# Kernel optimization log

Hardware: AMD Instinct MI355X
Metric: run time of the kernel (lower is better)

Reference implementation:

```python
import jax, jax.numpy as jnp
import numpy as np

N = 40000
IN_DIM = 2000
HID = 512
OUT_DIM = 30
E = 400000


def setup_inputs() -> dict:
    key = jax.random.key(0)
    k1, k2, k3, k4, k5, k6 = jax.random.split(key, 6)
    features = jax.random.normal(k1, (N, IN_DIM), dtype=jnp.float32)
    edge_index = jax.random.randint(k2, (2, E), 0, N, dtype=jnp.int64)
    # xavier_normal_(gain=1.414): std = gain * sqrt(2/(fan_in+fan_out))
    W1 = jax.random.normal(k3, (IN_DIM, HID), dtype=jnp.float32) * (1.414 * np.sqrt(2.0 / (IN_DIM + HID)))
    W2 = jax.random.normal(k4, (HID, OUT_DIM), dtype=jnp.float32) * (1.414 * np.sqrt(2.0 / (HID + OUT_DIM)))
    att_src = jax.random.normal(k5, (HID,), dtype=jnp.float32) * (1.414 * np.sqrt(2.0 / (1 + HID)))
    att_dst = jax.random.normal(k6, (HID,), dtype=jnp.float32) * (1.414 * np.sqrt(2.0 / (1 + HID)))
    return {"features": features, "W1": W1, "W2": W2,
            "att_src": att_src, "att_dst": att_dst, "edge_index": edge_index}


def _gat_propagate(x_proj, alpha_src, alpha_dst, src, dst, n_nodes):
    """GATConv message+aggregate (heads=1, aggr='add').
    x_proj: [N, C] projected features; alpha_src/alpha_dst: [N] per-node scores.
    """
    score = jax.nn.sigmoid(alpha_src[src] + alpha_dst[dst])          # [E]
    # segment softmax over destination neighborhoods (PyG softmax)
    seg_max = jax.ops.segment_max(score, dst, num_segments=n_nodes)  # [N]
    e = jnp.exp(score - seg_max[dst])                                # [E]
    seg_sum = jax.ops.segment_sum(e, dst, num_segments=n_nodes)     # [N]
    alpha = e / (seg_sum[dst] + 1e-16)                               # [E]
    msg = x_proj[src] * alpha[:, None]                               # [E, C] gather + scale
    return jax.ops.segment_sum(msg, dst, num_segments=n_nodes)      # [N, C] scatter-add


def _stagate_forward(features, W1, W2, att_src, att_dst, src, dst):
    n = features.shape[0]
    # conv1: attention=True (computes its own alpha)
    x1 = features @ W1                                # [N, HID]
    a_src = x1 @ att_src                              # [N]
    a_dst = x1 @ att_dst                              # [N]
    h1 = jax.nn.elu(_gat_propagate(x1, a_src, a_dst, src, dst, n))
    # conv2: attention=False -> just linear projection (heads=1 mean)
    h2 = h1 @ W2                                      # [N, OUT_DIM]
    # conv3: weights tied to W2^T, attention tied to conv1's alphas
    x3 = h2 @ W2.T                                    # [N, HID]
    h3 = jax.nn.elu(_gat_propagate(x3, a_src, a_dst, src, dst, n))
    # conv4: attention=False, weights tied to W1^T
    h4 = h3 @ W1.T                                    # [N, IN_DIM]
    return h2, h4


def reference(features, W1, W2, att_src, att_dst, edge_index):
    src = edge_index[0]
    dst = edge_index[1]
    return _stagate_forward(features, W1, W2, att_src, att_dst, src, dst)
```

## Files before the change

kernel.cpp:

```cpp
#include <hip/hip_runtime.h>
#include <cstdint>

#define NNODES 40000
#define INDIM 2000
#define HIDD 512
#define ODIM 30
#define NEDGES 400000
#define KPAD 2048

typedef short bf16x8 __attribute__((ext_vector_type(8)));
typedef float f32x4 __attribute__((ext_vector_type(4)));

__device__ __forceinline__ float bf2f(ushort u){ union{unsigned int i; float f;} x; x.i = ((unsigned int)u)<<16; return x.f; }
__device__ __forceinline__ ushort f2bf(float v){ union{float f; unsigned int u;} x; x.f=v; unsigned int r = x.u + 0x7fffu + ((x.u>>16)&1u); return (ushort)(r>>16); }

__device__ __forceinline__ int xcd_swz(int orig, int nwg){
  int q = nwg >> 3, r = nwg & 7;
  int xcd = orig & 7;
  int idx = orig >> 3;
  return (xcd < r ? xcd*(q+1) : r*(q+1) + (xcd-r)*q) + idx;
}

#define SB_FEAT   40000
#define SB_W1     (SB_FEAT + 4000)
#define SB_W2     (SB_W1 + 64)
#define SB_HIST   (SB_W2 + 1563)
#define SB_PAD    (SB_HIST + 96)
#define SB_CUR    (SB_PAD + 157)

__global__ __launch_bounds__(256) void setup_kernel(
    const float* __restrict__ features, const float* __restrict__ W1, const float* __restrict__ W2,
    const int* __restrict__ edst,
    ushort* __restrict__ featb, ushort* __restrict__ W1b, ushort* __restrict__ W1t,
    ushort* __restrict__ W2p, ushort* __restrict__ W2tc,
    int* __restrict__ deg, int* __restrict__ cursor){
  int b = blockIdx.x, t = threadIdx.x;
  if (b < SB_FEAT){
    int c = b*256 + t;
    int row = c >> 8, kc = c & 255;
    bf16x8 o;
    if (kc < INDIM/8) {
      const float* p = features + (size_t)row*INDIM + kc*8;
      #pragma unroll
      for (int j=0;j<8;++j) o[j] = (short)f2bf(p[j]);
    } else {
      #pragma unroll
      for (int j=0;j<8;++j) o[j] = 0;
    }
    *(bf16x8*)(featb + (size_t)row*KPAD + kc*8) = o;
  } else if (b < SB_W1){
    int idx = (b - SB_FEAT)*256 + t;
    int r = idx >> 9, c = idx & 511;
    ushort bb = f2bf(W1[idx]);
    W1b[idx] = bb;
    W1t[(size_t)c*KPAD + r] = bb;
  } else if (b < SB_W2){
    int idx = (b - SB_W1)*256 + t;
    int k = idx >> 5, c = idx & 31;
    float val = (c < ODIM) ? W2[k*ODIM + c] : 0.f;
    ushort bb = f2bf(val);
    W2p[k*32 + c] = bb;
    W2tc[c*HIDD + k] = bb;
  } else if (b < SB_HIST){
    int e = (b - SB_W2)*256 + t;
    if (e < NEDGES) atomicAdd(&deg[edst[e]], 1);
  } else if (b < SB_PAD){
    int z = (b - SB_HIST)*256 + t;
    int c = z / 48, r = 2000 + (z - c*48);
    W1t[(size_t)c*KPAD + r] = 0;
  } else {
    int z = (b - SB_PAD)*256 + t;
    if (z < NNODES) cursor[z] = 0;
  }
}

#define P_MID  asm volatile("" ::: "memory"); __builtin_amdgcn_s_barrier(); \
               asm volatile("s_waitcnt lgkmcnt(0)" ::: "memory"); \
               __builtin_amdgcn_sched_barrier(0); __builtin_amdgcn_s_setprio(1);
#define P_END  __builtin_amdgcn_s_setprio(0); asm volatile("" ::: "memory"); \
               __builtin_amdgcn_s_barrier(); __builtin_amdgcn_sched_barrier(0);
#define P_ENDW __builtin_amdgcn_s_setprio(0); \
               asm volatile("s_waitcnt vmcnt(4)" ::: "memory"); \
               asm volatile("" ::: "memory"); __builtin_amdgcn_s_barrier(); \
               __builtin_amdgcn_sched_barrier(0);

template<typename OutT, bool DOSCAN>
__global__ __launch_bounds__(512, 2) void gemm8_kernel(
    const ushort* __restrict__ A, const ushort* __restrict__ Bt,
    OutT* __restrict__ C, int M, int N, int K, int ldc, int nwg, int cshift,
    const int* __restrict__ degp, int* __restrict__ row_ptr)
{
  __shared__ __align__(16) char smem[131072];
  if constexpr (DOSCAN){
    if ((int)blockIdx.x == nwg){
      int* part = (int*)smem;
      const int t = threadIdx.x;
      const int base = t * 80;
      int s = 0;
      for (int j=0;j<80;++j){ int i = base+j; s += (i < NNODES) ? degp[i] : 0; }
      part[t] = s;
      __syncthreads();
      for (int off=1; off<512; off<<=1){
        int x = (t >= off) ? part[t-off] : 0;
        __syncthreads();
        part[t] += x;
        __syncthreads();
      }
      int run = (t > 0) ? part[t-1] : 0;
      for (int j=0;j<80;++j){
        int i = base+j;
        if (i <= NNODES){
          row_ptr[i] = run;
          if (i < NNODES) run += degp[i];
        }
      }
      return;
    }
  }
  ushort* Al = (ushort*)smem;
  ushort* Bl = (ushort*)(smem + 65536);
  const int tid = threadIdx.x;
  const int lane = tid & 63;
  const int w = tid >> 6;
  const int wm = w >> 2, wn = w & 3;
  const int s = xcd_swz(blockIdx.x, nwg);
  const int row0 = (s >> cshift) << 8;
  const int col0 = (s & ((1 << cshift) - 1)) << 8;
  const int NT = K >> 6;

  f32x4 acc[8][4] = {};
  bf16x8 a[4][2], b[4][2];

  auto stage = [&](bool isA, int kt, int h){
    const ushort* G = isA ? A : Bt;
    int base = isA ? row0 : col0;
    int lim  = isA ? M : N;
    ushort* L = (isA ? Al : Bl) + ((kt & 1) << 14);
    if (kt >= NT) kt -= NT;
    #pragma unroll
    for (int it = 0; it < 2; ++it){
      int ch = tid + (it << 9);
      int rl = (h << 7) + (ch >> 3);
      int cs = ch & 7;
      int gr = base + rl; gr = gr < lim ? gr : lim - 1;
      int gc = (kt << 6) + ((cs ^ (rl & 7)) << 3);
      __builtin_amdgcn_global_load_lds(
        (const __attribute__((address_space(1))) unsigned int*)(G + (size_t)gr*K + gc),
        (__attribute__((address_space(3))) unsigned int*)(L + rl*64 + cs*8), 16, 0, 0);
    }
  };
  auto lda = [&](int buf, int mf, int kk) -> bf16x8 {
    int rl = wm*128 + mf*16 + (lane & 15);
    int ko = kk*32 + ((lane >> 4) << 3);
    return *(const bf16x8*)&Al[(buf << 14) + rl*64 + (ko ^ ((rl & 7) << 3))];
  };
  auto ldb = [&](int buf, int nf, int kk) -> bf16x8 {
    int rl = wn*64 + nf*16 + (lane & 15);
    int ko = kk*32 + ((lane >> 4) << 3);
    return *(const bf16x8*)&Bl[(buf << 14) + rl*64 + (ko ^ ((rl & 7) << 3))];
  };
  auto mfma_q = [&](int mbase, int nbase){
    #pragma unroll
    for (int i=0;i<4;++i)
      #pragma unroll
      for (int j=0;j<2;++j)
        #pragma unroll
        for (int kk=0;kk<2;++kk)
          acc[mbase+i][nbase+j] = __builtin_amdgcn_mfma_f32_16x16x32_bf16(
              a[i][kk], b[nbase+j][kk], acc[mbase+i][nbase+j], 0, 0, 0);
  };

  stage(false, 0, 0); stage(false, 0, 1);
  stage(true , 0, 0); stage(true , 0, 1);
  stage(false, 1, 0); stage(false, 1, 1);
  asm volatile("s_waitcnt vmcnt(4)" ::: "memory");
  asm volatile("" ::: "memory");
  __builtin_amdgcn_s_barrier();
  __builtin_amdgcn_sched_barrier(0);

  const int NT2 = NT >> 1;
  for (int t = 0; t < NT2; ++t){
    const int kt0 = 2*t, kt1 = 2*t + 1;
    #pragma unroll
    for (int i=0;i<4;++i){ a[i][0]=lda(0,i,0); a[i][1]=lda(0,i,1); }
    #pragma unroll
    for (int j=0;j<2;++j){ b[j][0]=ldb(0,j,0); b[j][1]=ldb(0,j,1); }
    stage(true, kt1, 0);
    P_MID; mfma_q(0,0); P_END;
    #pragma unroll
    for (int j=2;j<4;++j){ b[j][0]=ldb(0,j,0); b[j][1]=ldb(0,j,1); }
    stage(true, kt1, 1);
    P_MID; mfma_q(0,2); P_END;
    #pragma unroll
    for (int i=0;i<4;++i){ a[i][0]=lda(0,4+i,0); a[i][1]=lda(0,4+i,1); }
    stage(false, kt0+2, 0);
    P_MID; mfma_q(4,0); P_END;
    stage(false, kt0+2, 1);
    P_MID; mfma_q(4,2); P_ENDW;
    #pragma unroll
    for (int i=0;i<4;++i){ a[i][0]=lda(1,i,0); a[i][1]=lda(1,i,1); }
    #pragma unroll
    for (int j=0;j<2;++j){ b[j][0]=ldb(1,j,0); b[j][1]=ldb(1,j,1); }
    stage(true, kt0+2, 0);
    P_MID; mfma_q(0,0); P_END;
    #pragma unroll
    for (int j=2;j<4;++j){ b[j][0]=ldb(1,j,0); b[j][1]=ldb(1,j,1); }
    stage(true, kt0+2, 1);
    P_MID; mfma_q(0,2); P_END;
    #pragma unroll
    for (int i=0;i<4;++i){ a[i][0]=lda(1,4+i,0); a[i][1]=lda(1,4+i,1); }
    stage(false, kt1+2, 0);
    P_MID; mfma_q(4,0); P_END;
    stage(false, kt1+2, 1);
    P_MID; mfma_q(4,2); P_ENDW;
  }

  asm volatile("s_waitcnt vmcnt(0)" ::: "memory");
  __syncthreads();

  if constexpr (sizeof(OutT)==2) {
    ushort* cs = (ushort*)smem;
    #pragma unroll
    for (int p=0;p<2;++p){
      if (wm == p){
        #pragma unroll
        for (int mf=0;mf<8;++mf)
          #pragma unroll
          for (int nf=0;nf<4;++nf)
            #pragma unroll
            for (int reg=0;reg<4;++reg)
              cs[(mf*16 + ((lane>>4)<<2) + reg)*264 + wn*64 + nf*16 + (lane&15)] = f2bf(acc[mf][nf][reg]);
      }
      __syncthreads();
      #pragma unroll
      for (int it=0; it<8; ++it){
        int ch = tid + it*512;
        int r = ch >> 5, c8 = (ch & 31) * 8;
        int gr = row0 + p*128 + r;
        if (gr < M && col0 + c8 + 8 <= N)
          *(bf16x8*)&((ushort*)C)[(size_t)gr*ldc + col0 + c8] = *(const bf16x8*)&cs[r*264 + c8];
      }
      __syncthreads();
    }
  } else {
    float* cf = (float*)smem;
    #pragma unroll
    for (int p=0;p<4;++p){
      if (wm == (p>>1)){
        int mh = (p & 1) * 4;
        #pragma unroll
        for (int i=0;i<4;++i)
          #pragma unroll
          for (int nf=0;nf<4;++nf)
            #pragma unroll
            for (int reg=0;reg<4;++reg)
              cf[(i*16 + ((lane>>4)<<2) + reg)*260 + wn*64 + nf*16 + (lane&15)] = acc[mh+i][nf][reg];
      }
      __syncthreads();
      #pragma unroll
      for (int it=0; it<8; ++it){
        int ch = tid + it*512;
        int r = ch >> 6, c4 = (ch & 63) * 4;
        int gr = row0 + p*64 + r, gc = col0 + c4;
        if (gr < M && gc + 4 <= N)
          *(f32x4*)&((float*)C)[(size_t)gr*ldc + gc] = *(const f32x4*)&cf[r*260 + c4];
      }
      __syncthreads();
    }
  }
}

#define PB_PLACE 1563
__global__ __launch_bounds__(256) void place_a_kernel(
    const int* __restrict__ esrc, const int* __restrict__ edst,
    const int* __restrict__ row_ptr, int* __restrict__ cursor, int* __restrict__ csr_src,
    const ushort* __restrict__ x1, const float* __restrict__ att_src, const float* __restrict__ att_dst,
    float* __restrict__ a_src, float* __restrict__ a_dst){
  int b = blockIdx.x, t = threadIdx.x;
  if (b < PB_PLACE){
    int e = b*256 + t;
    if (e >= NEDGES) return;
    int d = edst[e];
    int pos = row_ptr[d] + atomicAdd(&cursor[d], 1);
    csr_src[pos] = esrc[e];
  } else {
    int gid = (b - PB_PLACE)*256 + t;
    int row = gid >> 6, lane = gid & 63;
    if (row >= NNODES) return;
    bf16x8 v = *(const bf16x8*)(x1 + (size_t)row*HIDD + lane*8);
    float ps = 0.f, pd = 0.f;
    #pragma unroll
    for (int j=0;j<8;++j){
      float xv = bf2f((ushort)v[j]);
      ps += xv * att_src[lane*8+j];
      pd += xv * att_dst[lane*8+j];
    }
    #pragma unroll
    for (int off=32; off>0; off>>=1){ ps += __shfl_down(ps, off); pd += __shfl_down(pd, off); }
    if (lane == 0){ a_src[row] = ps; a_dst[row] = pd; }
  }
}

__global__ __launch_bounds__(256) void agg1_kernel(const ushort* __restrict__ X,
    const int* __restrict__ row_ptr, const int* __restrict__ csr_src,
    const float* __restrict__ a_src, const float* __restrict__ a_dst,
    float* __restrict__ csr_alpha, ushort* __restrict__ outb){
  int gid = blockIdx.x*256 + threadIdx.x;
  int v = gid >> 6, lane = gid & 63;
  if (v >= NNODES) return;
  int p0 = row_ptr[v], p1 = row_ptr[v+1], deg = p1 - p0;
  float ad = a_dst[v];
  float acc[8] = {0.f,0.f,0.f,0.f,0.f,0.f,0.f,0.f};

  if (deg > 0 && deg <= 64){
    bool act = lane < deg;
    int sv = act ? csr_src[p0 + lane] : 0;
    float sc = act ? 1.f/(1.f + __expf(-(a_src[sv] + ad))) : -1e30f;
    float m = sc;
    #pragma unroll
    for (int off=32; off>0; off>>=1) m = fmaxf(m, __shfl_xor(m, off));
    float e = act ? __expf(sc - m) : 0.f;
    float S = e;
    #pragma unroll
    for (int off=32; off>0; off>>=1) S += __shfl_xor(S, off);
    float al = e / (S + 1e-16f);
    if (act) csr_alpha[p0 + lane] = al;
    for (int j=0;j<deg;++j){
      float aj = __shfl(al, j);
      int sj = __shfl(sv, j);
      bf16x8 xv = *(const bf16x8*)(X + (size_t)sj*HIDD + lane*8);
      #pragma unroll
      for (int k=0;k<8;++k) acc[k] += aj * bf2f((ushort)xv[k]);
    }
  } else if (deg > 64){
    float m = -1e30f;
    for (int p = p0 + lane; p < p1; p += 64){
      float sc = 1.f/(1.f + __expf(-(a_src[csr_src[p]] + ad)));
      m = fmaxf(m, sc);
    }
    #pragma unroll
    for (int off=32; off>0; off>>=1) m = fmaxf(m, __shfl_xor(m, off));
    float S = 0.f;
    for (int p = p0 + lane; p < p1; p += 64){
      float sc = 1.f/(1.f + __expf(-(a_src[csr_src[p]] + ad)));
      S += __expf(sc - m);
    }
    #pragma unroll
    for (int off=32; off>0; off>>=1) S += __shfl_xor(S, off);
    float inv = 1.f/(S + 1e-16f);
    for (int base = p0; base < p1; base += 64){
      int p = base + lane;
      bool act = p < p1;
      int sv = act ? csr_src[p] : 0;
      float al = act ? __expf(1.f/(1.f + __expf(-(a_src[sv] + ad))) - m) * inv : 0.f;
      if (act) csr_alpha[p] = al;
      int cnt = p1 - base; cnt = cnt < 64 ? cnt : 64;
      for (int j=0;j<cnt;++j){
        float aj = __shfl(al, j);
        int sj = __shfl(sv, j);
        bf16x8 xv = *(const bf16x8*)(X + (size_t)sj*HIDD + lane*8);
        #pragma unroll
        for (int k=0;k<8;++k) acc[k] += aj * bf2f((ushort)xv[k]);
      }
    }
  }
  bf16x8 o;
  #pragma unroll
  for (int k=0;k<8;++k){
    float a = acc[k];
    a = a > 0.f ? a : __expf(a)-1.f;
    o[k] = (short)f2bf(a);
  }
  *(bf16x8*)(outb + (size_t)v*HIDD + lane*8) = o;
}

__global__ __launch_bounds__(256) void mid_kernel(const ushort* __restrict__ h1,
    const ushort* __restrict__ W2tc, float* __restrict__ h2){
  __shared__ ushort h1s[32*512];
  __shared__ ushort w2s[32*512];
  const int t = threadIdx.x;
  const int row0 = blockIdx.x * 32;
  const ushort* g = h1 + (size_t)row0*HIDD;
  #pragma unroll
  for (int it=0; it<8; ++it){
    int ch = t + it*256;
    *(bf16x8*)&h1s[ch*8] = *(const bf16x8*)&g[ch*8];
    *(bf16x8*)&w2s[ch*8] = *(const bf16x8*)&W2tc[ch*8];
  }
  __syncthreads();
  int c = t & 31, rg = t >> 5;
  if (c < ODIM){
    float acc[4] = {0.f,0.f,0.f,0.f};
    for (int k0=0;k0<64;++k0){
      bf16x8 wv = *(const bf16x8*)&w2s[c*512 + k0*8];
      #pragma unroll
      for (int rr=0; rr<4; ++rr){
        bf16x8 hv = *(const bf16x8*)&h1s[(rg*4+rr)*HIDD + k0*8];
        #pragma unroll
        for (int j=0;j<8;++j) acc[rr] += bf2f((ushort)hv[j]) * bf2f((ushort)wv[j]);
      }
    }
    #pragma unroll
    for (int rr=0;rr<4;++rr) h2[(size_t)(row0 + rg*4 + rr)*ODIM + c] = acc[rr];
  }
}

__global__ __launch_bounds__(256) void conv3_kernel(const float* __restrict__ h2,
    const int* __restrict__ row_ptr, const int* __restrict__ csr_src,
    const float* __restrict__ csr_alpha, const ushort* __restrict__ W2p,
    ushort* __restrict__ h3){
  int gid = blockIdx.x*256 + threadIdx.x;
  int v = gid >> 6, lane = gid & 63;
  if (v >= NNODES) return;
  int p0 = row_ptr[v], p1 = row_ptr[v+1];
  float accd = 0.f;
  if (lane < ODIM){
    for (int p = p0; p < p1; ++p)
      accd += csr_alpha[p] * h2[(size_t)csr_src[p]*ODIM + lane];
  }
  float gv[ODIM];
  #pragma unroll
  for (int ci=0; ci<ODIM; ++ci) gv[ci] = __shfl(accd, ci);
  #pragma unroll
  for (int it=0; it<8; ++it){
    int n = it*64 + lane;
    const ushort* wr = W2p + n*32;
    bf16x8 wvv[4];
    #pragma unroll
    for (int q=0;q<4;++q) wvv[q] = *(const bf16x8*)(wr + q*8);
    float acc = 0.f;
    #pragma unroll
    for (int ci=0; ci<ODIM; ++ci) acc += gv[ci]*bf2f((ushort)wvv[ci>>3][ci&7]);
    acc = acc > 0.f ? acc : __expf(acc)-1.f;
    h3[(size_t)v*HIDD + n] = f2bf(acc);
  }
}

extern "C" void kernel_launch(void* const* d_in, const int* in_sizes, int n_in,
                              void* d_out, int out_size, void* d_ws, size_t ws_size,
                              hipStream_t stream){
  const float* features = (const float*)d_in[0];
  const float* W1 = (const float*)d_in[1];
  const float* W2 = (const float*)d_in[2];
  const float* att_src = (const float*)d_in[3];
  const float* att_dst = (const float*)d_in[4];
  const int* edge = (const int*)d_in[5];
  const int* esrc = edge;
  const int* edst = edge + NEDGES;

  float* h2 = (float*)d_out;
  float* h4 = h2 + (size_t)NNODES*ODIM;
  char* obase = (char*)h4;
  ushort* featb = (ushort*)obase;
  ushort* x1b   = (ushort*)(obase + 163840000);
  ushort* h1b   = (ushort*)(obase + 204800000);

  char* wbase = (char*)d_ws;
  size_t o = 0;
  auto walloc = [&](size_t bytes)->void*{ void* p = wbase + o; o += (bytes + 255) & ~(size_t)255; return p; };
  ushort* h3b      = (ushort*)walloc((size_t)NNODES*HIDD*2);
  ushort* W1b      = (ushort*)walloc((size_t)INDIM*HIDD*2);
  ushort* W1t      = (ushort*)walloc((size_t)HIDD*KPAD*2);
  ushort* W2p      = (ushort*)walloc(512*32*2);
  ushort* W2tc     = (ushort*)walloc(32*512*2);
  float*  a_src    = (float*)walloc(NNODES*4);
  float*  a_dst    = (float*)walloc(NNODES*4);
  int*    deg      = (int*)walloc(NNODES*4);
  int*    cursor   = (int*)walloc(NNODES*4);
  int*    row_ptr  = (int*)walloc((NNODES+1)*4);
  int*    csr_src  = (int*)walloc(NEDGES*4);
  float*  csr_alpha= (float*)walloc(NEDGES*4);

  hipMemsetAsync(deg, 0, NNODES*4, stream);

  setup_kernel<<<SB_CUR, 256, 0, stream>>>(features, W1, W2, edst,
      featb, W1b, W1t, W2p, W2tc, deg, cursor);

  gemm8_kernel<ushort, true><<<315, 512, 0, stream>>>(featb, W1t, x1b,
      NNODES, HIDD, KPAD, HIDD, 314, 1, deg, row_ptr);

  place_a_kernel<<<PB_PLACE + 10000, 256, 0, stream>>>(esrc, edst,
      row_ptr, cursor, csr_src, x1b, att_src, att_dst, a_src, a_dst);

  agg1_kernel<<<10000, 256, 0, stream>>>(x1b, row_ptr, csr_src, a_src, a_dst, csr_alpha, h1b);
  mid_kernel<<<NNODES/32, 256, 0, stream>>>(h1b, W2tc, h2);
  conv3_kernel<<<10000, 256, 0, stream>>>(h2, row_ptr, csr_src, csr_alpha, W2p, h3b);
  gemm8_kernel<float, false><<<1256, 512, 0, stream>>>(h3b, W1b, h4,
      NNODES, INDIM, HIDD, INDIM, 1256, 3, nullptr, nullptr);
}
```

Measured before the change: 646.3 us.

## Fuse fp32-to-bf16 feature conversion into first GEMM's A-tile loads

Removes the separate pass that converted the 40000x2000 fp32 feature matrix into a padded bf16 copy. The first GEMM now loads fp32 A tiles into registers, converts them with packed bf16 conversion instructions, and writes them swizzled into LDS, with extra waitcnt and barriers woven into the pipelined loop. This avoids writing and re-reading a 160MB intermediate, at the cost of register-staged loads that no longer use direct global-to-LDS transfers and extra synchronisation inside the MFMA pipeline.

Result: slower. 873.7 us (+35.2%).

```diff
diff --git a/kernel.cpp b/kernel.cpp
--- a/kernel.cpp
+++ b/kernel.cpp
@@ -21,35 +21,21 @@
   return (xcd < r ? xcd*(q+1) : r*(q+1) + (xcd-r)*q) + idx;
 }
 
-#define SB_FEAT   40000
-#define SB_W1     (SB_FEAT + 4000)
+#define SB_W1     4000
 #define SB_W2     (SB_W1 + 64)
 #define SB_HIST   (SB_W2 + 1563)
 #define SB_PAD    (SB_HIST + 96)
 #define SB_CUR    (SB_PAD + 157)
 
 __global__ __launch_bounds__(256) void setup_kernel(
-    const float* __restrict__ features, const float* __restrict__ W1, const float* __restrict__ W2,
+    const float* __restrict__ W1, const float* __restrict__ W2,
     const int* __restrict__ edst,
-    ushort* __restrict__ featb, ushort* __restrict__ W1b, ushort* __restrict__ W1t,
+    ushort* __restrict__ W1b, ushort* __restrict__ W1t,
     ushort* __restrict__ W2p, ushort* __restrict__ W2tc,
     int* __restrict__ deg, int* __restrict__ cursor){
   int b = blockIdx.x, t = threadIdx.x;
-  if (b < SB_FEAT){
-    int c = b*256 + t;
-    int row = c >> 8, kc = c & 255;
-    bf16x8 o;
-    if (kc < INDIM/8) {
-      const float* p = features + (size_t)row*INDIM + kc*8;
-      #pragma unroll
-      for (int j=0;j<8;++j) o[j] = (short)f2bf(p[j]);
-    } else {
-      #pragma unroll
-      for (int j=0;j<8;++j) o[j] = 0;
-    }
-    *(bf16x8*)(featb + (size_t)row*KPAD + kc*8) = o;
-  } else if (b < SB_W1){
-    int idx = (b - SB_FEAT)*256 + t;
+  if (b < SB_W1){
+    int idx = b*256 + t;
     int r = idx >> 9, c = idx & 511;
     ushort bb = f2bf(W1[idx]);
     W1b[idx] = bb;
@@ -77,6 +63,11 @@
 #define P_MID  asm volatile("" ::: "memory"); __builtin_amdgcn_s_barrier(); \
                asm volatile("s_waitcnt lgkmcnt(0)" ::: "memory"); \
                __builtin_amdgcn_sched_barrier(0); __builtin_amdgcn_s_setprio(1);
+#define P_MIDW asm volatile("s_waitcnt lgkmcnt(0)" ::: "memory"); \
+               __builtin_amdgcn_sched_barrier(0); \
+               asm volatile("" ::: "memory"); __builtin_amdgcn_s_barrier(); \
+               asm volatile("s_waitcnt lgkmcnt(0)" ::: "memory"); \
+               __builtin_amdgcn_sched_barrier(0); __builtin_amdgcn_s_setprio(1);
 #define P_END  __builtin_amdgcn_s_setprio(0); asm volatile("" ::: "memory"); \
                __builtin_amdgcn_s_barrier(); __builtin_amdgcn_sched_barrier(0);
 #define P_ENDW __builtin_amdgcn_s_setprio(0); \
@@ -84,9 +75,9 @@
                asm volatile("" ::: "memory"); __builtin_amdgcn_s_barrier(); \
                __builtin_amdgcn_sched_barrier(0);
 
-template<typename OutT, bool DOSCAN>
+template<typename OutT, bool DOSCAN, bool AF32>
 __global__ __launch_bounds__(512, 2) void gemm8_kernel(
-    const ushort* __restrict__ A, const ushort* __restrict__ Bt,
+    const void* __restrict__ Aptr, const ushort* __restrict__ Bt,
     OutT* __restrict__ C, int M, int N, int K, int ldc, int nwg, int cshift,
     const int* __restrict__ degp, int* __restrict__ row_ptr)
 {
@@ -117,6 +108,8 @@
       return;
     }
   }
+  const ushort* Ab = (const ushort*)Aptr;
+  const float*  Af = (const float*)Aptr;
   ushort* Al = (ushort*)smem;
   ushort* Bl = (ushort*)(smem + 65536);
   const int tid = threadIdx.x;
@@ -130,9 +123,10 @@
 
   f32x4 acc[8][4] = {};
   bf16x8 a[4][2], b[4][2];
+  f32x4 sa0[4], sa1[4];
 
   auto stage = [&](bool isA, int kt, int h){
-    const ushort* G = isA ? A : Bt;
+    const ushort* G = isA ? Ab : Bt;
     int base = isA ? row0 : col0;
     int lim  = isA ? M : N;
     ushort* L = (isA ? Al : Bl) + ((kt & 1) << 14);
@@ -147,6 +141,41 @@
       __builtin_amdgcn_global_load_lds(
         (const __attribute__((address_space(1))) unsigned int*)(G + (size_t)gr*K + gc),
         (__attribute__((address_space(3))) unsigned int*)(L + rl*64 + cs*8), 16, 0, 0);
+    }
+  };
+
+  auto a_issue = [&](int kt, int h, f32x4* sr){
+    if (kt >= NT) kt -= NT;
+    #pragma unroll
+    for (int u = 0; u < 2; ++u){
+      int ch = u*1024 + tid*2;
+      int rl = (h << 7) + (ch >> 4);
+      int q0 = ch & 15;
+      int gr = row0 + rl; gr = gr < M ? gr : M - 1;
+      int k0 = (kt << 6) + q0*4;
+      bool ok0 = k0 < INDIM, ok1 = (k0 + 4) < INDIM;
+      const float* rp = Af + (size_t)gr*INDIM;
+      f32x4 t0 = *(const f32x4*)(rp + (ok0 ? k0 : 0));
+      f32x4 t1 = *(const f32x4*)(rp + (ok1 ? k0 + 4 : 0));
+      f32x4 z = {0.f,0.f,0.f,0.f};
+      sr[u*2]   = ok0 ? t0 : z;
+      sr[u*2+1] = ok1 ? t1 : z;
+    }
+  };
+  auto a_write = [&](int kt, int h, const f32x4* sr){
+    ushort* L = Al + ((kt & 1) << 14);
+    #pragma unroll
+    for (int u = 0; u < 2; ++u){
+      int ch = u*1024 + tid*2;
+      int rl = (h << 7) + (ch >> 4);
+      int sl = (ch & 15) >> 1;
+      const f32x4 lo = sr[u*2], hi = sr[u*2+1];
+      union { bf16x8 v; unsigned uu[4]; } r;
+      asm("v_cvt_pk_bf16_f32 %0, %1, %2" : "=v"(r.uu[0]) : "v"(lo[0]), "v"(lo[1]));
+      asm("v_cvt_pk_bf16_f32 %0, %1, %2" : "=v"(r.uu[1]) : "v"(lo[2]), "v"(lo[3]));
+      asm("v_cvt_pk_bf16_f32 %0, %1, %2" : "=v"(r.uu[2]) : "v"(hi[0]), "v"(hi[1]));
+      asm("v_cvt_pk_bf16_f32 %0, %1, %2" : "=v"(r.uu[3]) : "v"(hi[2]), "v"(hi[3]));
+      *(bf16x8*)&L[rl*64 + ((sl ^ (rl & 7)) << 3)] = r.v;
     }
   };
   auto lda = [&](int buf, int mf, int kk) -> bf16x8 {
@@ -170,13 +199,26 @@
               a[i][kk], b[nbase+j][kk], acc[mbase+i][nbase+j], 0, 0, 0);
   };
 
-  stage(false, 0, 0); stage(false, 0, 1);
-  stage(true , 0, 0); stage(true , 0, 1);
-  stage(false, 1, 0); stage(false, 1, 1);
-  asm volatile("s_waitcnt vmcnt(4)" ::: "memory");
-  asm volatile("" ::: "memory");
-  __builtin_amdgcn_s_barrier();
-  __builtin_amdgcn_sched_barrier(0);
+  if constexpr (AF32){
+    a_issue(0, 0, sa0); a_issue(0, 1, sa1);
+    stage(false, 0, 0); stage(false, 0, 1);
+    stage(false, 1, 0); stage(false, 1, 1);
+    asm volatile("s_waitcnt vmcnt(8)" ::: "memory");
+    __builtin_amdgcn_sched_barrier(0);
+    a_write(0, 0, sa0); a_write(0, 1, sa1);
+    asm volatile("s_waitcnt vmcnt(4) lgkmcnt(0)" ::: "memory");
+    asm volatile("" ::: "memory");
+    __builtin_amdgcn_s_barrier();
+    __builtin_amdgcn_sched_barrier(0);
+  } else {
+    stage(false, 0, 0); stage(false, 0, 1);
+    stage(true , 0, 0); stage(true , 0, 1);
+    stage(false, 1, 0); stage(false, 1, 1);
+    asm volatile("s_waitcnt vmcnt(4)" ::: "memory");
+    asm volatile("" ::: "memory");
+    __builtin_amdgcn_s_barrier();
+    __builtin_amdgcn_sched_barrier(0);
+  }
 
   const int NT2 = NT >> 1;
   for (int t = 0; t < NT2; ++t){
@@ -185,34 +227,62 @@
     for (int i=0;i<4;++i){ a[i][0]=lda(0,i,0); a[i][1]=lda(0,i,1); }
     #pragma unroll
     for (int j=0;j<2;++j){ b[j][0]=ldb(0,j,0); b[j][1]=ldb(0,j,1); }
-    stage(true, kt1, 0);
+    if constexpr (AF32) a_issue(kt1, 0, sa0); else stage(true, kt1, 0);
     P_MID; mfma_q(0,0); P_END;
     #pragma unroll
     for (int j=2;j<4;++j){ b[j][0]=ldb(0,j,0); b[j][1]=ldb(0,j,1); }
-    stage(true, kt1, 1);
+    if constexpr (AF32) a_issue(kt1, 1, sa1); else stage(true, kt1, 1);
     P_MID; mfma_q(0,2); P_END;
     #pragma unroll
     for (int i=0;i<4;++i){ a[i][0]=lda(0,4+i,0); a[i][1]=lda(0,4+i,1); }
     stage(false, kt0+2, 0);
-    P_MID; mfma_q(4,0); P_END;
+    if constexpr (AF32){
+      asm volatile("s_waitcnt vmcnt(6)" ::: "memory");
+      __builtin_amdgcn_sched_barrier(0);
+      a_write(kt1, 0, sa0);
+      P_MIDW; mfma_q(4,0); P_END;
+    } else {
+      P_MID; mfma_q(4,0); P_END;
+    }
     stage(false, kt0+2, 1);
-    P_MID; mfma_q(4,2); P_ENDW;
+    if constexpr (AF32){
+      asm volatile("s_waitcnt vmcnt(4)" ::: "memory");
+      __builtin_amdgcn_sched_barrier(0);
+      a_write(kt1, 1, sa1);
+      P_MIDW; mfma_q(4,2); P_END;
+    } else {
+      P_MID; mfma_q(4,2); P_ENDW;
+    }
     #pragma unroll
     for (int i=0;i<4;++i){ a[i][0]=lda(1,i,0); a[i][1]=lda(1,i,1); }
     #pragma unroll
     for (int j=0;j<2;++j){ b[j][0]=ldb(1,j,0); b[j][1]=ldb(1,j,1); }
-    stage(true, kt0+2, 0);
+    if constexpr (AF32) a_issue(kt0+2, 0, sa0); else stage(true, kt0+2, 0);
     P_MID; mfma_q(0,0); P_END;
     #pragma unroll
     for (int j=2;j<4;++j){ b[j][0]=ldb(1,j,0); b[j][1]=ldb(1,j,1); }
-    stage(true, kt0+2, 1);
+    if constexpr (AF32) a_issue(kt0+2, 1, sa1); else stage(true, kt0+2, 1);
     P_MID; mfma_q(0,2); P_END;
     #pragma unroll
     for (int i=0;i<4;++i){ a[i][0]=lda(1,4+i,0); a[i][1]=lda(1,4+i,1); }
     stage(false, kt1+2, 0);
-    P_MID; mfma_q(4,0); P_END;
+    if constexpr (AF32){
+      asm volatile("s_waitcnt vmcnt(6)" ::: "memory");
+      __builtin_amdgcn_sched_barrier(0);
+      a_write(kt0+2, 0, sa0);
+      P_MIDW; mfma_q(4,0); P_END;
+    } else {
+      P_MID; mfma_q(4,0); P_END;
+    }
     stage(false, kt1+2, 1);
-    P_MID; mfma_q(4,2); P_ENDW;
+    if constexpr (AF32){
+      asm volatile("s_waitcnt vmcnt(4)" ::: "memory");
+      __builtin_amdgcn_sched_barrier(0);
+      a_write(kt0+2, 1, sa1);
+      P_MIDW; mfma_q(4,2); P_END;
+    } else {
+      P_MID; mfma_q(4,2); P_ENDW;
+    }
   }
 
   asm volatile("s_waitcnt vmcnt(0)" ::: "memory");
@@ -451,7 +521,6 @@
   float* h2 = (float*)d_out;
   float* h4 = h2 + (size_t)NNODES*ODIM;
   char* obase = (char*)h4;
-  ushort* featb = (ushort*)obase;
   ushort* x1b   = (ushort*)(obase + 163840000);
   ushort* h1b   = (ushort*)(obase + 204800000);
 
@@ -473,10 +542,10 @@
 
   hipMemsetAsync(deg, 0, NNODES*4, stream);
 
-  setup_kernel<<<SB_CUR, 256, 0, stream>>>(features, W1, W2, edst,
-      featb, W1b, W1t, W2p, W2tc, deg, cursor);
-
-  gemm8_kernel<ushort, true><<<315, 512, 0, stream>>>(featb, W1t, x1b,
+  setup_kernel<<<SB_CUR, 256, 0, stream>>>(W1, W2, edst,
+      W1b, W1t, W2p, W2tc, deg, cursor);
+
+  gemm8_kernel<ushort, true, true><<<315, 512, 0, stream>>>((const void*)features, W1t, x1b,
       NNODES, HIDD, KPAD, HIDD, 314, 1, deg, row_ptr);
 
   place_a_kernel<<<PB_PLACE + 10000, 256, 0, stream>>>(esrc, edst,
@@ -485,6 +554,6 @@
   agg1_kernel<<<10000, 256, 0, stream>>>(x1b, row_ptr, csr_src, a_src, a_dst, csr_alpha, h1b);
   mid_kernel<<<NNODES/32, 256, 0, stream>>>(h1b, W2tc, h2);
   conv3_kernel<<<10000, 256, 0, stream>>>(h2, row_ptr, csr_src, csr_alpha, W2p, h3b);
-  gemm8_kernel<float, false><<<1256, 512, 0, stream>>>(h3b, W1b, h4,
+  gemm8_kernel<float, false, false><<<1256, 512, 0, stream>>>((const void*)h3b, W1b, h4,
       NNODES, INDIM, HIDD, INDIM, 1256, 3, nullptr, nullptr);
 }
```

## Split first GEMM in two halves to overlap casting, scan and CSR placement

Applied to the files above, without the earlier changes.

The features cast is split: setup casts only the first 20224 rows, and the first GEMM half runs alongside the scan and the cast of the remaining rows in one launch. The second GEMM half shares a launch with CSR edge placement and the attention dot products for the first half of the rows. A small kernel then computes attention scores for the second half. The aim is to hide memory-bound cast and graph-build work behind tensor-core GEMM blocks, at the cost of an extra launch and mixed-role grids competing for CUs.

Measured after the change: 620.4 us. 4.0% less time.

```diff
diff --git a/kernel.cpp b/kernel.cpp
--- a/kernel.cpp
+++ b/kernel.cpp
@@ -7,6 +7,7 @@
 #define ODIM 30
 #define NEDGES 400000
 #define KPAD 2048
+#define ROWSPLIT 20224
 
 typedef short bf16x8 __attribute__((ext_vector_type(8)));
 typedef float f32x4 __attribute__((ext_vector_type(4)));
@@ -19,59 +20,6 @@
   int xcd = orig & 7;
   int idx = orig >> 3;
   return (xcd < r ? xcd*(q+1) : r*(q+1) + (xcd-r)*q) + idx;
-}
-
-#define SB_FEAT   40000
-#define SB_W1     (SB_FEAT + 4000)
-#define SB_W2     (SB_W1 + 64)
-#define SB_HIST   (SB_W2 + 1563)
-#define SB_PAD    (SB_HIST + 96)
-#define SB_CUR    (SB_PAD + 157)
-
-__global__ __launch_bounds__(256) void setup_kernel(
-    const float* __restrict__ features, const float* __restrict__ W1, const float* __restrict__ W2,
-    const int* __restrict__ edst,
-    ushort* __restrict__ featb, ushort* __restrict__ W1b, ushort* __restrict__ W1t,
-    ushort* __restrict__ W2p, ushort* __restrict__ W2tc,
-    int* __restrict__ deg, int* __restrict__ cursor){
-  int b = blockIdx.x, t = threadIdx.x;
-  if (b < SB_FEAT){
-    int c = b*256 + t;
-    int row = c >> 8, kc = c & 255;
-    bf16x8 o;
-    if (kc < INDIM/8) {
-      const float* p = features + (size_t)row*INDIM + kc*8;
-      #pragma unroll
-      for (int j=0;j<8;++j) o[j] = (short)f2bf(p[j]);
-    } else {
-      #pragma unroll
-      for (int j=0;j<8;++j) o[j] = 0;
-    }
-    *(bf16x8*)(featb + (size_t)row*KPAD + kc*8) = o;
-  } else if (b < SB_W1){
-    int idx = (b - SB_FEAT)*256 + t;
-    int r = idx >> 9, c = idx & 511;
-    ushort bb = f2bf(W1[idx]);
-    W1b[idx] = bb;
-    W1t[(size_t)c*KPAD + r] = bb;
-  } else if (b < SB_W2){
-    int idx = (b - SB_W1)*256 + t;
-    int k = idx >> 5, c = idx & 31;
-    float val = (c < ODIM) ? W2[k*ODIM + c] : 0.f;
-    ushort bb = f2bf(val);
-    W2p[k*32 + c] = bb;
-    W2tc[c*HIDD + k] = bb;
-  } else if (b < SB_HIST){
-    int e = (b - SB_W2)*256 + t;
-    if (e < NEDGES) atomicAdd(&deg[edst[e]], 1);
-  } else if (b < SB_PAD){
-    int z = (b - SB_HIST)*256 + t;
-    int c = z / 48, r = 2000 + (z - c*48);
-    W1t[(size_t)c*KPAD + r] = 0;
-  } else {
-    int z = (b - SB_PAD)*256 + t;
-    if (z < NNODES) cursor[z] = 0;
-  }
 }
 
 #define P_MID  asm volatile("" ::: "memory"); __builtin_amdgcn_s_barrier(); \
@@ -84,48 +32,18 @@
                asm volatile("" ::: "memory"); __builtin_amdgcn_s_barrier(); \
                __builtin_amdgcn_sched_barrier(0);
 
-template<typename OutT, bool DOSCAN>
-__global__ __launch_bounds__(512, 2) void gemm8_kernel(
+template<typename OutT>
+__device__ __forceinline__ void gemm_body(
     const ushort* __restrict__ A, const ushort* __restrict__ Bt,
-    OutT* __restrict__ C, int M, int N, int K, int ldc, int nwg, int cshift,
-    const int* __restrict__ degp, int* __restrict__ row_ptr)
+    OutT* __restrict__ C, int M, int N, int K, int ldc,
+    int row0, int col0, char* smem)
 {
-  __shared__ __align__(16) char smem[131072];
-  if constexpr (DOSCAN){
-    if ((int)blockIdx.x == nwg){
-      int* part = (int*)smem;
-      const int t = threadIdx.x;
-      const int base = t * 80;
-      int s = 0;
-      for (int j=0;j<80;++j){ int i = base+j; s += (i < NNODES) ? degp[i] : 0; }
-      part[t] = s;
-      __syncthreads();
-      for (int off=1; off<512; off<<=1){
-        int x = (t >= off) ? part[t-off] : 0;
-        __syncthreads();
-        part[t] += x;
-        __syncthreads();
-      }
-      int run = (t > 0) ? part[t-1] : 0;
-      for (int j=0;j<80;++j){
-        int i = base+j;
-        if (i <= NNODES){
-          row_ptr[i] = run;
-          if (i < NNODES) run += degp[i];
-        }
-      }
-      return;
-    }
-  }
   ushort* Al = (ushort*)smem;
   ushort* Bl = (ushort*)(smem + 65536);
   const int tid = threadIdx.x;
   const int lane = tid & 63;
   const int w = tid >> 6;
   const int wm = w >> 2, wn = w & 3;
-  const int s = xcd_swz(blockIdx.x, nwg);
-  const int row0 = (s >> cshift) << 8;
-  const int col0 = (s & ((1 << cshift) - 1)) << 8;
   const int NT = K >> 6;
 
   f32x4 acc[8][4] = {};
@@ -270,23 +188,133 @@
   }
 }
 
-#define PB_PLACE 1563
-__global__ __launch_bounds__(256) void place_a_kernel(
+__device__ __forceinline__ void cast_rows2(const float* __restrict__ features,
+    ushort* __restrict__ featb, int row_base, int cb){
+  int t = threadIdx.x;
+  int row = row_base + (cb<<1) + (t>>8);
+  int kc = t & 255;
+  bf16x8 o;
+  if (kc < INDIM/8) {
+    const float* p = features + (size_t)row*INDIM + kc*8;
+    #pragma unroll
+    for (int j=0;j<8;++j) o[j] = (short)f2bf(p[j]);
+  } else {
+    #pragma unroll
+    for (int j=0;j<8;++j) o[j] = 0;
+  }
+  *(bf16x8*)(featb + (size_t)row*KPAD + kc*8) = o;
+}
+
+__device__ __forceinline__ void scan_body(const int* __restrict__ degp,
+    int* __restrict__ row_ptr, int* part){
+  const int t = threadIdx.x;
+  const int base = t * 80;
+  int s = 0;
+  for (int j=0;j<80;++j){ int i = base+j; s += (i < NNODES) ? degp[i] : 0; }
+  part[t] = s;
+  __syncthreads();
+  for (int off=1; off<512; off<<=1){
+    int x = (t >= off) ? part[t-off] : 0;
+    __syncthreads();
+    part[t] += x;
+    __syncthreads();
+  }
+  int run = (t > 0) ? part[t-1] : 0;
+  for (int j=0;j<80;++j){
+    int i = base+j;
+    if (i <= NNODES){
+      row_ptr[i] = run;
+      if (i < NNODES) run += degp[i];
+    }
+  }
+}
+
+#define S1_CAST   10112
+#define S1_W1     (S1_CAST + 2000)
+#define S1_W2     (S1_W1 + 32)
+#define S1_HIST   (S1_W2 + 782)
+#define S1_PAD    (S1_HIST + 48)
+#define S1_CUR    (S1_PAD + 79)
+
+__global__ __launch_bounds__(512) void setup_kernel(
+    const float* __restrict__ features, const float* __restrict__ W1, const float* __restrict__ W2,
+    const int* __restrict__ edst,
+    ushort* __restrict__ featb, ushort* __restrict__ W1b, ushort* __restrict__ W1t,
+    ushort* __restrict__ W2p, ushort* __restrict__ W2tc,
+    int* __restrict__ deg, int* __restrict__ cursor){
+  int b = blockIdx.x, t = threadIdx.x;
+  if (b < S1_CAST){
+    cast_rows2(features, featb, 0, b);
+  } else if (b < S1_W1){
+    int idx = (b - S1_CAST)*512 + t;
+    int r = idx >> 9, c = idx & 511;
+    ushort bb = f2bf(W1[idx]);
+    W1b[idx] = bb;
+    W1t[(size_t)c*KPAD + r] = bb;
+  } else if (b < S1_W2){
+    int idx = (b - S1_W1)*512 + t;
+    int k = idx >> 5, c = idx & 31;
+    float val = (c < ODIM) ? W2[k*ODIM + c] : 0.f;
+    ushort bb = f2bf(val);
+    W2p[k*32 + c] = bb;
+    W2tc[c*HIDD + k] = bb;
+  } else if (b < S1_HIST){
+    int e = (b - S1_W2)*512 + t;
+    if (e < NEDGES) atomicAdd(&deg[edst[e]], 1);
+  } else if (b < S1_PAD){
+    int z = (b - S1_HIST)*512 + t;
+    int c = z / 48, r = 2000 + (z - c*48);
+    W1t[(size_t)c*KPAD + r] = 0;
+  } else {
+    int z = (b - S1_PAD)*512 + t;
+    if (z < NNODES) cursor[z] = 0;
+  }
+}
+
+#define K2_G 158
+__global__ __launch_bounds__(512, 2) void gemm1a_kernel(
+    const ushort* __restrict__ featb, const ushort* __restrict__ W1t, ushort* __restrict__ x1,
+    const float* __restrict__ features, ushort* __restrict__ featb_w,
+    const int* __restrict__ deg, int* __restrict__ row_ptr){
+  __shared__ __align__(16) char smem[131072];
+  int b = blockIdx.x;
+  if (b < K2_G){
+    int s = xcd_swz(b, K2_G);
+    int row0 = (s >> 1) << 8;
+    int col0 = (s & 1) << 8;
+    gemm_body<ushort>(featb, W1t, x1, NNODES, HIDD, KPAD, HIDD, row0, col0, smem);
+  } else if (b == K2_G){
+    scan_body(deg, row_ptr, (int*)smem);
+  } else {
+    cast_rows2(features, featb_w, ROWSPLIT, b - K2_G - 1);
+  }
+}
+
+#define K3_G 156
+#define K3_PL (K3_G + 782)
+__global__ __launch_bounds__(512, 2) void gemm1b_kernel(
+    const ushort* __restrict__ featb, const ushort* __restrict__ W1t, ushort* __restrict__ x1,
     const int* __restrict__ esrc, const int* __restrict__ edst,
     const int* __restrict__ row_ptr, int* __restrict__ cursor, int* __restrict__ csr_src,
-    const ushort* __restrict__ x1, const float* __restrict__ att_src, const float* __restrict__ att_dst,
+    const float* __restrict__ att_src, const float* __restrict__ att_dst,
     float* __restrict__ a_src, float* __restrict__ a_dst){
+  __shared__ __align__(16) char smem[131072];
   int b = blockIdx.x, t = threadIdx.x;
-  if (b < PB_PLACE){
-    int e = b*256 + t;
-    if (e >= NEDGES) return;
-    int d = edst[e];
-    int pos = row_ptr[d] + atomicAdd(&cursor[d], 1);
-    csr_src[pos] = esrc[e];
+  if (b < K3_G){
+    int s = xcd_swz(b, K3_G);
+    int row0 = ROWSPLIT + ((s >> 1) << 8);
+    int col0 = (s & 1) << 8;
+    gemm_body<ushort>(featb, W1t, x1, NNODES, HIDD, KPAD, HIDD, row0, col0, smem);
+  } else if (b < K3_PL){
+    int e = (b - K3_G)*512 + t;
+    if (e < NEDGES){
+      int d = edst[e];
+      int pos = row_ptr[d] + atomicAdd(&cursor[d], 1);
+      csr_src[pos] = esrc[e];
+    }
   } else {
-    int gid = (b - PB_PLACE)*256 + t;
+    int gid = (b - K3_PL)*512 + t;
     int row = gid >> 6, lane = gid & 63;
-    if (row >= NNODES) return;
     bf16x8 v = *(const bf16x8*)(x1 + (size_t)row*HIDD + lane*8);
     float ps = 0.f, pd = 0.f;
     #pragma unroll
@@ -299,6 +327,37 @@
     for (int off=32; off>0; off>>=1){ ps += __shfl_down(ps, off); pd += __shfl_down(pd, off); }
     if (lane == 0){ a_src[row] = ps; a_dst[row] = pd; }
   }
+}
+
+__global__ __launch_bounds__(512) void a2_kernel(const ushort* __restrict__ x1,
+    const float* __restrict__ att_src, const float* __restrict__ att_dst,
+    float* __restrict__ a_src, float* __restrict__ a_dst){
+  int gid = blockIdx.x*512 + threadIdx.x;
+  int row = ROWSPLIT + (gid >> 6), lane = gid & 63;
+  if (row >= NNODES) return;
+  bf16x8 v = *(const bf16x8*)(x1 + (size_t)row*HIDD + lane*8);
+  float ps = 0.f, pd = 0.f;
+  #pragma unroll
+  for (int j=0;j<8;++j){
+    float xv = bf2f((ushort)v[j]);
+    ps += xv * att_src[lane*8+j];
+    pd += xv * att_dst[lane*8+j];
+  }
+  #pragma unroll
+  for (int off=32; off>0; off>>=1){ ps += __shfl_down(ps, off); pd += __shfl_down(pd, off); }
+  if (lane == 0){ a_src[row] = ps; a_dst[row] = pd; }
+}
+
+template<typename OutT>
+__global__ __launch_bounds__(512, 2) void gemm8_kernel(
+    const ushort* __restrict__ A, const ushort* __restrict__ Bt,
+    OutT* __restrict__ C, int M, int N, int K, int ldc, int nwg, int cshift)
+{
+  __shared__ __align__(16) char smem[131072];
+  int s = xcd_swz(blockIdx.x, nwg);
+  int row0 = (s >> cshift) << 8;
+  int col0 = (s & ((1 << cshift) - 1)) << 8;
+  gemm_body<OutT>(A, Bt, C, M, N, K, ldc, row0, col0, smem);
 }
 
 __global__ __launch_bounds__(256) void agg1_kernel(const ushort* __restrict__ X,
@@ -473,18 +532,20 @@
 
   hipMemsetAsync(deg, 0, NNODES*4, stream);
 
-  setup_kernel<<<SB_CUR, 256, 0, stream>>>(features, W1, W2, edst,
+  setup_kernel<<<S1_CUR, 512, 0, stream>>>(features, W1, W2, edst,
       featb, W1b, W1t, W2p, W2tc, deg, cursor);
 
-  gemm8_kernel<ushort, true><<<315, 512, 0, stream>>>(featb, W1t, x1b,
-      NNODES, HIDD, KPAD, HIDD, 314, 1, deg, row_ptr);
-
-  place_a_kernel<<<PB_PLACE + 10000, 256, 0, stream>>>(esrc, edst,
-      row_ptr, cursor, csr_src, x1b, att_src, att_dst, a_src, a_dst);
+  gemm1a_kernel<<<K2_G + 1 + 9888, 512, 0, stream>>>(featb, W1t, x1b,
+      features, featb, deg, row_ptr);
+
+  gemm1b_kernel<<<K3_PL + 2528, 512, 0, stream>>>(featb, W1t, x1b,
+      esrc, edst, row_ptr, cursor, csr_src, att_src, att_dst, a_src, a_dst);
+
+  a2_kernel<<<2472, 512, 0, stream>>>(x1b, att_src, att_dst, a_src, a_dst);
 
   agg1_kernel<<<10000, 256, 0, stream>>>(x1b, row_ptr, csr_src, a_src, a_dst, csr_alpha, h1b);
   mid_kernel<<<NNODES/32, 256, 0, stream>>>(h1b, W2tc, h2);
   conv3_kernel<<<10000, 256, 0, stream>>>(h2, row_ptr, csr_src, csr_alpha, W2p, h3b);
-  gemm8_kernel<float, false><<<1256, 512, 0, stream>>>(h3b, W1b, h4,
-      NNODES, INDIM, HIDD, INDIM, 1256, 3, nullptr, nullptr);
-}
+  gemm8_kernel<float><<<1256, 512, 0, stream>>>(h3b, W1b, h4,
+      NNODES, INDIM, HIDD, INDIM, 1256, 3);
+}
```
